# Optimization experiments

Hardware: AMD Instinct MI355X
Metric: run time of the kernel (lower is better)

## Reference

```python
import jax, jax.numpy as jnp
import numpy as np

D_MODEL = 2048
N_HEADS = 16
KV_HEADS = 4
HEAD_DIM = D_MODEL // N_HEADS  # 128
B, T = 2, 2048


def setup_inputs() -> dict:
    key = jax.random.key(0)
    ks = jax.random.split(key, 8)
    s = 1.0 / np.sqrt(D_MODEL)
    x = jax.random.normal(ks[0], (B, T, D_MODEL), dtype=jnp.float32)
    # Linear weights stored as (in_features, out_features); y = x @ W
    Wq = jax.random.normal(ks[1], (D_MODEL, D_MODEL), dtype=jnp.float32) * s
    Wk = jax.random.normal(ks[2], (D_MODEL, KV_HEADS * HEAD_DIM), dtype=jnp.float32) * s
    Wv = jax.random.normal(ks[3], (D_MODEL, KV_HEADS * HEAD_DIM), dtype=jnp.float32) * s
    Wo = jax.random.normal(ks[4], (D_MODEL, D_MODEL), dtype=jnp.float32) * s
    weight_logits = jnp.ones((KV_HEADS,), dtype=jnp.float32)
    weight_values = jnp.ones((KV_HEADS,), dtype=jnp.float32)
    # additive causal mask (1, 1, T, T): 0 on/below diag, -inf above
    neg_inf = jnp.float32(-1e30)
    causal = jnp.tril(jnp.ones((T, T), dtype=bool))
    attn_mask = jnp.where(causal, jnp.float32(0.0), neg_inf)[None, None]
    return {"x": x, "attn_mask": attn_mask, "Wq": Wq, "Wk": Wk, "Wv": Wv,
            "Wo": Wo, "weight_logits": weight_logits, "weight_values": weight_values}


def reference(x, attn_mask, Wq, Wk, Wv, Wo, weight_logits, weight_values):
    Bx, Tx, _ = x.shape
    H, G, D = N_HEADS, KV_HEADS, HEAD_DIM
    group_size = H // G
    head_to_group = jnp.arange(H) // group_size  # (H,)

    q = (x @ Wq).reshape(Bx, Tx, H, D).transpose(0, 2, 1, 3)  # (B,H,T,D)
    k = (x @ Wk).reshape(Bx, Tx, G, D).transpose(0, 2, 1, 3)  # (B,G,T,D)
    v = (x @ Wv).reshape(Bx, Tx, G, D).transpose(0, 2, 1, 3)  # (B,G,T,D)

    # GQA expansion: gather kv groups per head
    k_g = k[:, head_to_group]  # (B,H,T,D)
    v_g = v[:, head_to_group]  # (B,H,T,D)
    # (use_value_weight=False: weight_values unused)

    logit_scale = weight_logits[head_to_group][None, :, None, None]  # (1,H,1,1)
    inv_sqrt_d = jnp.float32(1.0 / np.sqrt(D))
    logits = jnp.einsum('bhqd,bhkd->bhqk', q, k_g) * inv_sqrt_d * logit_scale
    logits = logits + attn_mask
    attn = jax.nn.softmax(logits, axis=-1)  # dropout p=0 -> identity
    y = jnp.einsum('bhqk,bhkd->bhqd', attn, v_g)
    y = y.transpose(0, 2, 1, 3).reshape(Bx, Tx, H * D)
    return y @ Wo
```

## Files before the change

kernel.cpp:

```cpp
#include <hip/hip_runtime.h>
#include <hip/hip_bf16.h>

#define TT 2048
#define DM 2048
#define NH 16
#define KVH 4
#define HD 128

typedef __attribute__((ext_vector_type(8))) short bs8;
typedef __attribute__((ext_vector_type(4))) float fx4;
typedef __attribute__((ext_vector_type(4))) unsigned short us4;
typedef __attribute__((ext_vector_type(8))) unsigned short us8;

#if __has_builtin(__builtin_amdgcn_exp2f)
#define EXP2(x) __builtin_amdgcn_exp2f(x)
#else
#define EXP2(x) exp2f(x)
#endif

__device__ inline unsigned short f2b(float f) {
  __hip_bfloat16 h = __float2bfloat16(f);
  return *reinterpret_cast<unsigned short*>(&h);
}

__device__ inline float b2f(unsigned short u) {
  unsigned int v = ((unsigned int)u) << 16;
  return *reinterpret_cast<float*>(&v);
}

__device__ inline void gld_lds16(const ushort* g, ushort* l) {
  __builtin_amdgcn_global_load_lds(
      (const __attribute__((address_space(1))) void*)g,
      (__attribute__((address_space(3))) void*)l,
      16, 0, 0);
}

__global__ __launch_bounds__(256) void prep_kernel(
    const float* __restrict__ x, const float* __restrict__ Wq,
    const float* __restrict__ Wk, const float* __restrict__ Wv,
    const float* __restrict__ Wo, ushort* __restrict__ xb,
    ushort* __restrict__ Wqkvt, ushort* __restrict__ Wot) {
  int tx = threadIdx.x, ty = threadIdx.y;
  if (blockIdx.z == 2) {
    int lin = (blockIdx.y * 96 + blockIdx.x) * 256 + ty * 32 + tx;
#pragma unroll
    for (int it = 0; it < 2; ++it) {
      int i = lin + it * (6144 * 256);
      if (i < (TT * 2 * DM) / 4) {
        float4 v = ((const float4*)x)[i];
        us4 o = {f2b(v.x), f2b(v.y), f2b(v.z), f2b(v.w)};
        ((us4*)xb)[i] = o;
      }
    }
    return;
  }
  __shared__ float t[32][33];
  int n0 = blockIdx.x * 32, k0 = blockIdx.y * 32;
  if (blockIdx.z == 0) {
    const float* src;
    int srcN, col0;
    if (n0 < 2048) { src = Wq; srcN = 2048; col0 = n0; }
    else if (n0 < 2560) { src = Wk; srcN = 512; col0 = n0 - 2048; }
    else { src = Wv; srcN = 512; col0 = n0 - 2560; }
    for (int jj = 0; jj < 4; ++jj)
      t[ty + jj * 8][tx] = src[(size_t)(k0 + ty + jj * 8) * srcN + col0 + tx];
    __syncthreads();
    for (int jj = 0; jj < 4; ++jj)
      Wqkvt[(size_t)(n0 + ty + jj * 8) * 2048 + k0 + tx] = f2b(t[tx][ty + jj * 8]);
  } else {
    if (n0 >= 2048) return;
    for (int jj = 0; jj < 4; ++jj)
      t[ty + jj * 8][tx] = Wo[(size_t)(k0 + ty + jj * 8) * 2048 + n0 + tx];
    __syncthreads();
    for (int jj = 0; jj < 4; ++jj)
      Wot[(size_t)(n0 + ty + jj * 8) * 2048 + k0 + tx] = f2b(t[tx][ty + jj * 8]);
  }
}

#define EPI_STRIDE 136
__global__ __launch_bounds__(256) void gemm_qkv(const ushort* __restrict__ A,
                                                const ushort* __restrict__ Bt,
                                                ushort* __restrict__ qo,
                                                ushort* __restrict__ ko,
                                                ushort* __restrict__ vo,
                                                int K) {
  __shared__ alignas(16) ushort smem[128 * EPI_STRIDE];
  ushort* As = smem;
  ushort* Bs = smem + 8192;
  const int tid = threadIdx.x;
  const int lane = tid & 63;
  const int wid = tid >> 6;
  const int wm = wid >> 1, wn = wid & 1;
  const int quad = lane >> 4, l16 = lane & 15;
  const int bm = blockIdx.y * 128, bn = blockIdx.x * 128;

  fx4 acc[4][4];
  for (int i = 0; i < 4; ++i)
    for (int j = 0; j < 4; ++j) acc[i][j] = (fx4){0.f, 0.f, 0.f, 0.f};

  const int r8 = lane >> 3, s8 = lane & 7;
  for (int k0 = 0; k0 < K; k0 += 64) {
    for (int i = 0; i < 4; ++i) {
      int m = i * 32 + wid * 8 + r8;
      int c = s8 ^ (m & 7);
      gld_lds16(A + (size_t)(bm + m) * K + k0 + c * 8, As + (i * 32 + wid * 8) * 64);
      gld_lds16(Bt + (size_t)(bn + m) * K + k0 + c * 8, Bs + (i * 32 + wid * 8) * 64);
    }
    __syncthreads();
    for (int ks = 0; ks < 2; ++ks) {
      bs8 af[4], bf[4];
      for (int mt = 0; mt < 4; ++mt) {
        int m = wm * 64 + mt * 16 + l16;
        int c = ks * 4 + quad;
        int slot = c ^ (m & 7);
        af[mt] = *(const bs8*)(As + m * 64 + slot * 8);
      }
      for (int nt = 0; nt < 4; ++nt) {
        int n = wn * 64 + nt * 16 + l16;
        int c = ks * 4 + quad;
        int slot = c ^ (n & 7);
        bf[nt] = *(const bs8*)(Bs + n * 64 + slot * 8);
      }
      for (int mt = 0; mt < 4; ++mt)
        for (int nt = 0; nt < 4; ++nt)
          acc[mt][nt] = __builtin_amdgcn_mfma_f32_16x16x32_bf16(af[mt], bf[nt],
                                                                acc[mt][nt], 0, 0, 0);
    }
    __syncthreads();
  }

  for (int mt = 0; mt < 4; ++mt)
    for (int nt = 0; nt < 4; ++nt)
      for (int r = 0; r < 4; ++r) {
        int row = wm * 64 + mt * 16 + quad * 4 + r;
        int col = wn * 64 + nt * 16 + l16;
        smem[row * EPI_STRIDE + col] = f2b(acc[mt][nt][r]);
      }
  __syncthreads();
  const int rsel = tid >> 4;
  const int csel = tid & 15;
  for (int ii = 0; ii < 8; ++ii) {
    int row = ii * 16 + rsel;
    us8 chunk = *(const us8*)(smem + row * EPI_STRIDE + csel * 8);
    int row_g = bm + row;
    int colc = bn + csel * 8;
    if (bn < 2048) {
      *(us8*)(qo + (size_t)row_g * 2048 + colc) = chunk;
    } else {
      int b = row_g >> 11, t = row_g & 2047;
      if (bn < 2560) {
        int kc = colc - 2048;
        int gg = kc >> 7, d = kc & 127;
        *(us8*)(ko + ((size_t)(b * KVH + gg) * TT + t) * HD + d) = chunk;
      } else {
        int vc = colc - 2560;
        int gg = vc >> 7, d = vc & 127;
        *(us8*)(vo + ((size_t)(b * KVH + gg) * TT + t) * HD + d) = chunk;
      }
    }
  }
}

__global__ __launch_bounds__(256) void transpose_v(const ushort* __restrict__ vin,
                                                   ushort* __restrict__ vout) {
  __shared__ ushort tl[32][33];
  int tx = threadIdx.x, ty = threadIdx.y;
  int t0 = blockIdx.x * 32, d0 = blockIdx.y * 32;
  size_t base = (size_t)blockIdx.z * TT * HD;
  for (int jj = 0; jj < 4; ++jj)
    tl[ty + jj * 8][tx] = vin[base + (size_t)(t0 + ty + jj * 8) * HD + d0 + tx];
  __syncthreads();
  for (int jj = 0; jj < 4; ++jj)
    vout[base + (size_t)(d0 + ty + jj * 8) * TT + t0 + tx] = tl[tx][ty + jj * 8];
}

__global__ __launch_bounds__(256) void gemm_out(const ushort* __restrict__ A,
                                                const ushort* __restrict__ Bt,
                                                float* __restrict__ Cout,
                                                int N, int K) {
  __shared__ alignas(16) ushort smem[128 * EPI_STRIDE];
  ushort* As = smem;
  ushort* Bs = smem + 8192;
  const int tid = threadIdx.x;
  const int lane = tid & 63;
  const int wid = tid >> 6;
  const int wm = wid >> 1, wn = wid & 1;
  const int quad = lane >> 4, l16 = lane & 15;
  const int bm = blockIdx.y * 128, bn = blockIdx.x * 128;

  fx4 acc[4][4];
  for (int i = 0; i < 4; ++i)
    for (int j = 0; j < 4; ++j) acc[i][j] = (fx4){0.f, 0.f, 0.f, 0.f};

  const int r8 = lane >> 3, s8 = lane & 7;
  for (int k0 = 0; k0 < K; k0 += 64) {
    for (int i = 0; i < 4; ++i) {
      int m = i * 32 + wid * 8 + r8;
      int c = s8 ^ (m & 7);
      gld_lds16(A + (size_t)(bm + m) * K + k0 + c * 8, As + (i * 32 + wid * 8) * 64);
      gld_lds16(Bt + (size_t)(bn + m) * K + k0 + c * 8, Bs + (i * 32 + wid * 8) * 64);
    }
    __syncthreads();
    for (int ks = 0; ks < 2; ++ks) {
      bs8 af[4], bf[4];
      for (int mt = 0; mt < 4; ++mt) {
        int m = wm * 64 + mt * 16 + l16;
        int c = ks * 4 + quad;
        int slot = c ^ (m & 7);
        af[mt] = *(const bs8*)(As + m * 64 + slot * 8);
      }
      for (int nt = 0; nt < 4; ++nt) {
        int n = wn * 64 + nt * 16 + l16;
        int c = ks * 4 + quad;
        int slot = c ^ (n & 7);
        bf[nt] = *(const bs8*)(Bs + n * 64 + slot * 8);
      }
      for (int mt = 0; mt < 4; ++mt)
        for (int nt = 0; nt < 4; ++nt)
          acc[mt][nt] = __builtin_amdgcn_mfma_f32_16x16x32_bf16(af[mt], bf[nt],
                                                                acc[mt][nt], 0, 0, 0);
    }
    __syncthreads();
  }

  for (int mt = 0; mt < 4; ++mt)
    for (int nt = 0; nt < 4; ++nt)
      for (int r = 0; r < 4; ++r) {
        int row = wm * 64 + mt * 16 + quad * 4 + r;
        int col = wn * 64 + nt * 16 + l16;
        smem[row * EPI_STRIDE + col] = f2b(acc[mt][nt][r]);
      }
  __syncthreads();
  const int rsel = tid >> 4;
  const int csel = tid & 15;
  for (int ii = 0; ii < 8; ++ii) {
    int row = ii * 16 + rsel;
    us8 chunk = *(const us8*)(smem + row * EPI_STRIDE + csel * 8);
    int row_g = bm + row;
    int colc = bn + csel * 8;
    float4 lo = {b2f(chunk[0]), b2f(chunk[1]), b2f(chunk[2]), b2f(chunk[3])};
    float4 hi = {b2f(chunk[4]), b2f(chunk[5]), b2f(chunk[6]), b2f(chunk[7])};
    *(float4*)(Cout + (size_t)row_g * N + colc) = lo;
    *(float4*)(Cout + (size_t)row_g * N + colc + 4) = hi;
  }
}

__global__ __launch_bounds__(512, 4) void attn_kernel(const ushort* __restrict__ qb,
                                                      const ushort* __restrict__ kb,
                                                      const ushort* __restrict__ vt,
                                                      ushort* __restrict__ yb,
                                                      const float* __restrict__ wlog) {
  __shared__ alignas(16) ushort Ks[2][64 * 128];
  __shared__ alignas(16) ushort Vs[2][128 * 64];
  __shared__ alignas(16) ushort Ps[128 * 64];

  const int bid = blockIdx.x;
  const int qt = (bid & 256) ? (bid & 15) : 15 - (bid & 15);
  const int h = (bid >> 4) & 15;
  const int b = bid >> 8;
  const int g = h >> 2;
  const int tid = threadIdx.x;
  const int lane = tid & 63;
  const int wid = tid >> 6;
  const int quad = lane >> 4;
  const int l16 = lane & 15;
  const int qw = qt * 128 + wid * 16;

  const float scale = wlog[g] * 0.08838834764831845f;
  const float sc2 = scale * 1.4426950408889634f;

  const ushort* kbase = kb + (size_t)(b * KVH + g) * TT * HD;
  const ushort* vbase = vt + (size_t)(b * KVH + g) * HD * TT;

  const ushort* kp;
  const ushort* vp;
  {
    int keyr = wid * 4 + (lane >> 4);
    int si = lane & 15;
    int ck = (si & 8) | ((si ^ keyr) & 7);
    kp = kbase + (size_t)keyr * HD + ck * 8;
    int dr = wid * 8 + (lane >> 3);
    int s8 = lane & 7;
    int cv = s8 ^ (dr & 7);
    vp = vbase + (size_t)dr * TT + cv * 8;
  }

  gld_lds16(kp, &Ks[0][wid * 512]);
  gld_lds16(kp + 32 * HD, &Ks[0][4096 + wid * 512]);
  gld_lds16(vp, &Vs[0][wid * 512]);
  gld_lds16(vp + 64 * TT, &Vs[0][4096 + wid * 512]);
  kp += 64 * HD;
  vp += 64;

  bs8 qf[4];
  {
    int q = qw + l16;
    const ushort* qrow = qb + ((size_t)(b * TT + q)) * DM + h * HD;
#pragma unroll
    for (int ks = 0; ks < 4; ++ks)
      qf[ks] = *(const bs8*)(qrow + ks * 32 + quad * 8);
  }

  float m_i = -INFINITY;
  float l_i = 0.f;
  fx4 o[8];
#pragma unroll
  for (int i = 0; i < 8; ++i) o[i] = (fx4){0.f, 0.f, 0.f, 0.f};

  const int jmax = 2 * qt + 1;
  for (int j = 0; j <= jmax; ++j) {
    const int cur = j & 1;
    if (j < jmax) {
      const int nxt = cur ^ 1;
      gld_lds16(kp, &Ks[nxt][wid * 512]);
      gld_lds16(kp + 32 * HD, &Ks[nxt][4096 + wid * 512]);
      gld_lds16(vp, &Vs[nxt][wid * 512]);
      gld_lds16(vp + 64 * TT, &Vs[nxt][4096 + wid * 512]);
      kp += 64 * HD;
      vp += 64;
      asm volatile("s_waitcnt vmcnt(4)" ::: "memory");
    } else {
      asm volatile("s_waitcnt vmcnt(0)" ::: "memory");
    }
    __builtin_amdgcn_s_barrier();

    if (j * 64 <= qw + 15) {
      const ushort* Kc = Ks[cur];
      const ushort* Vc = Vs[cur];
      fx4 s[4];
#pragma unroll
      for (int mt = 0; mt < 4; ++mt) s[mt] = (fx4){0.f, 0.f, 0.f, 0.f};
      __builtin_amdgcn_s_setprio(1);
#pragma unroll
      for (int mt = 0; mt < 4; ++mt) {
        bs8 a[4];
        int key = mt * 16 + l16;
#pragma unroll
        for (int ks = 0; ks < 4; ++ks) {
          int c = ks * 4 + quad;
          int slot = (c & 8) | ((c ^ key) & 7);
          a[ks] = *(const bs8*)(Kc + key * 128 + slot * 8);
        }
#pragma unroll
        for (int ks = 0; ks < 4; ++ks)
          s[mt] = __builtin_amdgcn_mfma_f32_16x16x32_bf16(a[ks], qf[ks],
                                                          s[mt], 0, 0, 0);
      }
      __builtin_amdgcn_s_setprio(0);

      const int q = qw + l16;
      if (j * 64 + 63 > qw) {
#pragma unroll
        for (int mt = 0; mt < 4; ++mt)
#pragma unroll
          for (int r = 0; r < 4; ++r) {
            int key = j * 64 + mt * 16 + quad * 4 + r;
            if (key > q) s[mt][r] = -1e30f;
          }
      }
      float mx = s[0][0];
#pragma unroll
      for (int mt = 0; mt < 4; ++mt)
#pragma unroll
        for (int r = 0; r < 4; ++r) mx = fmaxf(mx, s[mt][r]);
      mx = fmaxf(mx, __shfl_xor(mx, 16));
      mx = fmaxf(mx, __shfl_xor(mx, 32));

      if (!__all((mx - m_i) * scale <= 8.0f)) {
        float m_new = fmaxf(m_i, mx);
        float alpha = EXP2((m_i - m_new) * sc2);
        l_i *= alpha;
#pragma unroll
        for (int dmt = 0; dmt < 8; ++dmt)
#pragma unroll
          for (int r = 0; r < 4; ++r) o[dmt][r] *= alpha;
        m_i = m_new;
      }
      float negb = -m_i * sc2;
      float sum = 0.f;
#pragma unroll
      for (int mt = 0; mt < 4; ++mt)
#pragma unroll
        for (int r = 0; r < 4; ++r) {
          float pv = EXP2(fmaf(s[mt][r], sc2, negb));
          s[mt][r] = pv;
          sum += pv;
        }
      sum += __shfl_xor(sum, 16);
      sum += __shfl_xor(sum, 32);
      l_i += sum;

      int qrow = wid * 16 + l16;
      int sw = qrow & 7;
#pragma unroll
      for (int mt = 0; mt < 4; ++mt) {
        us4 pw = {f2b(s[mt][0]), f2b(s[mt][1]), f2b(s[mt][2]), f2b(s[mt][3])};
        int chunk = mt * 2 + (quad >> 1);
        *(us4*)(Ps + qrow * 64 + ((chunk ^ sw) << 3) + ((quad & 1) << 2)) = pw;
      }

#pragma unroll
      for (int ks = 0; ks < 2; ++ks) {
        bs8 pb = *(const bs8*)(Ps + qrow * 64 + (((ks * 4 + quad) ^ sw) << 3));
        __builtin_amdgcn_s_setprio(1);
#pragma unroll
        for (int dmt = 0; dmt < 8; ++dmt) {
          int d = dmt * 16 + l16;
          int c = ks * 4 + quad;
          int slot = c ^ (d & 7);
          bs8 va = *(const bs8*)(Vc + d * 64 + slot * 8);
          o[dmt] = __builtin_amdgcn_mfma_f32_16x16x32_bf16(va, pb, o[dmt], 0, 0, 0);
        }
        __builtin_amdgcn_s_setprio(0);
      }
    }
    asm volatile("s_waitcnt lgkmcnt(0)" ::: "memory");
    __builtin_amdgcn_s_barrier();
  }

  {
    float inv = 1.0f / l_i;
    int q = qw + l16;
    ushort* yrow = yb + ((size_t)(b * TT + q)) * DM + h * HD;
#pragma unroll
    for (int dmt = 0; dmt < 8; ++dmt) {
      us4 w = {f2b(o[dmt][0] * inv), f2b(o[dmt][1] * inv),
               f2b(o[dmt][2] * inv), f2b(o[dmt][3] * inv)};
      *(us4*)(yrow + dmt * 16 + quad * 4) = w;
    }
  }
}

extern "C" void kernel_launch(void* const* d_in, const int* in_sizes, int n_in,
                              void* d_out, int out_size, void* d_ws, size_t ws_size,
                              hipStream_t stream) {
  const float* x = (const float*)d_in[0];
  const float* Wq = (const float*)d_in[2];
  const float* Wk = (const float*)d_in[3];
  const float* Wv = (const float*)d_in[4];
  const float* Wo = (const float*)d_in[5];
  const float* wlog = (const float*)d_in[6];

  char* ws = (char*)d_ws;
  ushort* xb = (ushort*)ws;     ws += (size_t)4096 * 2048 * 2;
  ushort* Wqkvt = (ushort*)ws;  ws += (size_t)3072 * 2048 * 2;
  ushort* Wot = (ushort*)ws;    ws += (size_t)2048 * 2048 * 2;
  ushort* qbuf = (ushort*)ws;   ws += (size_t)4096 * 2048 * 2;
  ushort* kbuf = (ushort*)ws;   ws += (size_t)2 * KVH * 2048 * 128 * 2;
  ushort* vtmp = (ushort*)ws;   ws += (size_t)2 * KVH * 2048 * 128 * 2;
  ushort* vbuf = (ushort*)ws;   ws += (size_t)2 * KVH * 2048 * 128 * 2;
  ushort* ybuf = (ushort*)ws;   ws += (size_t)4096 * 2048 * 2;

  prep_kernel<<<dim3(96, 64, 3), dim3(32, 8), 0, stream>>>(
      x, Wq, Wk, Wv, Wo, xb, Wqkvt, Wot);
  gemm_qkv<<<dim3(24, 32), 256, 0, stream>>>(xb, Wqkvt, qbuf, kbuf, vtmp, 2048);
  transpose_v<<<dim3(64, 4, 8), dim3(32, 8), 0, stream>>>(vtmp, vbuf);
  attn_kernel<<<512, 512, 0, stream>>>(qbuf, kbuf, vbuf, ybuf, wlog);
  gemm_out<<<dim3(16, 32), 256, 0, stream>>>(ybuf, Wot, (float*)d_out, 2048, 2048);
}
```

Before: 301.8 us.

## Give each attention wave two 16-row query tiles to reuse K/V fragments

The attention kernel moves from 8 waves of 16 query rows each to 4 waves of 32 query rows each, so every K and V fragment read from LDS feeds two MFMAs. Each thread now issues twice as many global-to-LDS loads per tile, and the vmcnt wait is adjusted to match. LDS read traffic per MFMA drops, but register pressure roughly doubles for accumulators and scores. Occupancy changes with the new launch bounds, and each causal-diagonal tile now has coarser masking per wave.

```diff
diff --git a/kernel.cpp b/kernel.cpp
--- a/kernel.cpp
+++ b/kernel.cpp
@@ -245,7 +245,7 @@
   }
 }
 
-__global__ __launch_bounds__(512, 4) void attn_kernel(const ushort* __restrict__ qb,
+__global__ __launch_bounds__(256, 2) void attn_kernel(const ushort* __restrict__ qb,
                                                       const ushort* __restrict__ kb,
                                                       const ushort* __restrict__ vt,
                                                       ushort* __restrict__ yb,
@@ -264,7 +264,7 @@
   const int wid = tid >> 6;
   const int quad = lane >> 4;
   const int l16 = lane & 15;
-  const int qw = qt * 128 + wid * 16;
+  const int qwv = qt * 128 + wid * 32;
 
   const float scale = wlog[g] * 0.08838834764831845f;
   const float sc2 = scale * 1.4426950408889634f;
@@ -285,123 +285,151 @@
     vp = vbase + (size_t)dr * TT + cv * 8;
   }
 
-  gld_lds16(kp, &Ks[0][wid * 512]);
-  gld_lds16(kp + 32 * HD, &Ks[0][4096 + wid * 512]);
-  gld_lds16(vp, &Vs[0][wid * 512]);
-  gld_lds16(vp + 64 * TT, &Vs[0][4096 + wid * 512]);
+#pragma unroll
+  for (int r = 0; r < 4; ++r) {
+    gld_lds16(kp + (size_t)(16 * r) * HD, &Ks[0][r * 2048 + wid * 512]);
+    gld_lds16(vp + (size_t)(32 * r) * TT, &Vs[0][r * 2048 + wid * 512]);
+  }
   kp += 64 * HD;
   vp += 64;
 
-  bs8 qf[4];
-  {
-    int q = qw + l16;
+  bs8 qf[2][4];
+#pragma unroll
+  for (int nt = 0; nt < 2; ++nt) {
+    int q = qwv + nt * 16 + l16;
     const ushort* qrow = qb + ((size_t)(b * TT + q)) * DM + h * HD;
 #pragma unroll
     for (int ks = 0; ks < 4; ++ks)
-      qf[ks] = *(const bs8*)(qrow + ks * 32 + quad * 8);
-  }
-
-  float m_i = -INFINITY;
-  float l_i = 0.f;
-  fx4 o[8];
-#pragma unroll
-  for (int i = 0; i < 8; ++i) o[i] = (fx4){0.f, 0.f, 0.f, 0.f};
+      qf[nt][ks] = *(const bs8*)(qrow + ks * 32 + quad * 8);
+  }
+
+  float m_i[2] = {-INFINITY, -INFINITY};
+  float l_i[2] = {0.f, 0.f};
+  fx4 o[8][2];
+#pragma unroll
+  for (int i = 0; i < 8; ++i)
+#pragma unroll
+    for (int nt = 0; nt < 2; ++nt) o[i][nt] = (fx4){0.f, 0.f, 0.f, 0.f};
 
   const int jmax = 2 * qt + 1;
   for (int j = 0; j <= jmax; ++j) {
     const int cur = j & 1;
     if (j < jmax) {
       const int nxt = cur ^ 1;
-      gld_lds16(kp, &Ks[nxt][wid * 512]);
-      gld_lds16(kp + 32 * HD, &Ks[nxt][4096 + wid * 512]);
-      gld_lds16(vp, &Vs[nxt][wid * 512]);
-      gld_lds16(vp + 64 * TT, &Vs[nxt][4096 + wid * 512]);
+#pragma unroll
+      for (int r = 0; r < 4; ++r) {
+        gld_lds16(kp + (size_t)(16 * r) * HD, &Ks[nxt][r * 2048 + wid * 512]);
+        gld_lds16(vp + (size_t)(32 * r) * TT, &Vs[nxt][r * 2048 + wid * 512]);
+      }
       kp += 64 * HD;
       vp += 64;
-      asm volatile("s_waitcnt vmcnt(4)" ::: "memory");
+      asm volatile("s_waitcnt vmcnt(8)" ::: "memory");
     } else {
       asm volatile("s_waitcnt vmcnt(0)" ::: "memory");
     }
     __builtin_amdgcn_s_barrier();
 
-    if (j * 64 <= qw + 15) {
+    if (j * 64 <= qwv + 31) {
       const ushort* Kc = Ks[cur];
       const ushort* Vc = Vs[cur];
-      fx4 s[4];
-#pragma unroll
-      for (int mt = 0; mt < 4; ++mt) s[mt] = (fx4){0.f, 0.f, 0.f, 0.f};
+      fx4 s[4][2];
+#pragma unroll
+      for (int mt = 0; mt < 4; ++mt)
+#pragma unroll
+        for (int nt = 0; nt < 2; ++nt) s[mt][nt] = (fx4){0.f, 0.f, 0.f, 0.f};
       __builtin_amdgcn_s_setprio(1);
 #pragma unroll
       for (int mt = 0; mt < 4; ++mt) {
-        bs8 a[4];
         int key = mt * 16 + l16;
 #pragma unroll
         for (int ks = 0; ks < 4; ++ks) {
           int c = ks * 4 + quad;
           int slot = (c & 8) | ((c ^ key) & 7);
-          a[ks] = *(const bs8*)(Kc + key * 128 + slot * 8);
+          bs8 a = *(const bs8*)(Kc + key * 128 + slot * 8);
+          s[mt][0] = __builtin_amdgcn_mfma_f32_16x16x32_bf16(a, qf[0][ks],
+                                                             s[mt][0], 0, 0, 0);
+          s[mt][1] = __builtin_amdgcn_mfma_f32_16x16x32_bf16(a, qf[1][ks],
+                                                             s[mt][1], 0, 0, 0);
         }
-#pragma unroll
-        for (int ks = 0; ks < 4; ++ks)
-          s[mt] = __builtin_amdgcn_mfma_f32_16x16x32_bf16(a[ks], qf[ks],
-                                                          s[mt], 0, 0, 0);
       }
       __builtin_amdgcn_s_setprio(0);
 
-      const int q = qw + l16;
-      if (j * 64 + 63 > qw) {
+      if (j * 64 + 63 > qwv) {
+#pragma unroll
+        for (int nt = 0; nt < 2; ++nt) {
+          int q = qwv + nt * 16 + l16;
+#pragma unroll
+          for (int mt = 0; mt < 4; ++mt)
+#pragma unroll
+            for (int r = 0; r < 4; ++r) {
+              int key = j * 64 + mt * 16 + quad * 4 + r;
+              if (key > q) s[mt][nt][r] = -1e30f;
+            }
+        }
+      }
+      float mx[2];
+#pragma unroll
+      for (int nt = 0; nt < 2; ++nt) {
+        float m = s[0][nt][0];
 #pragma unroll
         for (int mt = 0; mt < 4; ++mt)
 #pragma unroll
+          for (int r = 0; r < 4; ++r) m = fmaxf(m, s[mt][nt][r]);
+        m = fmaxf(m, __shfl_xor(m, 16));
+        m = fmaxf(m, __shfl_xor(m, 32));
+        mx[nt] = m;
+      }
+
+      bool ok = ((mx[0] - m_i[0]) * scale <= 8.0f) &&
+                ((mx[1] - m_i[1]) * scale <= 8.0f);
+      if (!__all(ok)) {
+#pragma unroll
+        for (int nt = 0; nt < 2; ++nt) {
+          float m_new = fmaxf(m_i[nt], mx[nt]);
+          float alpha = EXP2((m_i[nt] - m_new) * sc2);
+          l_i[nt] *= alpha;
+#pragma unroll
+          for (int dmt = 0; dmt < 8; ++dmt)
+#pragma unroll
+            for (int r = 0; r < 4; ++r) o[dmt][nt][r] *= alpha;
+          m_i[nt] = m_new;
+        }
+      }
+#pragma unroll
+      for (int nt = 0; nt < 2; ++nt) {
+        float negb = -m_i[nt] * sc2;
+        float sum = 0.f;
+#pragma unroll
+        for (int mt = 0; mt < 4; ++mt)
+#pragma unroll
           for (int r = 0; r < 4; ++r) {
-            int key = j * 64 + mt * 16 + quad * 4 + r;
-            if (key > q) s[mt][r] = -1e30f;
+            float pv = EXP2(fmaf(s[mt][nt][r], sc2, negb));
+            s[mt][nt][r] = pv;
+            sum += pv;
           }
-      }
-      float mx = s[0][0];
-#pragma unroll
-      for (int mt = 0; mt < 4; ++mt)
-#pragma unroll
-        for (int r = 0; r < 4; ++r) mx = fmaxf(mx, s[mt][r]);
-      mx = fmaxf(mx, __shfl_xor(mx, 16));
-      mx = fmaxf(mx, __shfl_xor(mx, 32));
-
-      if (!__all((mx - m_i) * scale <= 8.0f)) {
-        float m_new = fmaxf(m_i, mx);
-        float alpha = EXP2((m_i - m_new) * sc2);
-        l_i *= alpha;
-#pragma unroll
-        for (int dmt = 0; dmt < 8; ++dmt)
-#pragma unroll
-          for (int r = 0; r < 4; ++r) o[dmt][r] *= alpha;
-        m_i = m_new;
-      }
-      float negb = -m_i * sc2;
-      float sum = 0.f;
-#pragma unroll
-      for (int mt = 0; mt < 4; ++mt)
-#pragma unroll
-        for (int r = 0; r < 4; ++r) {
-          float pv = EXP2(fmaf(s[mt][r], sc2, negb));
-          s[mt][r] = pv;
-          sum += pv;
+        sum += __shfl_xor(sum, 16);
+        sum += __shfl_xor(sum, 32);
+        l_i[nt] += sum;
+      }
+
+      const int sw = l16 & 7;
+#pragma unroll
+      for (int nt = 0; nt < 2; ++nt) {
+        int qrow = wid * 32 + nt * 16 + l16;
+#pragma unroll
+        for (int mt = 0; mt < 4; ++mt) {
+          us4 pw = {f2b(s[mt][nt][0]), f2b(s[mt][nt][1]),
+                    f2b(s[mt][nt][2]), f2b(s[mt][nt][3])};
+          int chunk = mt * 2 + (quad >> 1);
+          *(us4*)(Ps + qrow * 64 + ((chunk ^ sw) << 3) + ((quad & 1) << 2)) = pw;
         }
-      sum += __shfl_xor(sum, 16);
-      sum += __shfl_xor(sum, 32);
-      l_i += sum;
-
-      int qrow = wid * 16 + l16;
-      int sw = qrow & 7;
-#pragma unroll
-      for (int mt = 0; mt < 4; ++mt) {
-        us4 pw = {f2b(s[mt][0]), f2b(s[mt][1]), f2b(s[mt][2]), f2b(s[mt][3])};
-        int chunk = mt * 2 + (quad >> 1);
-        *(us4*)(Ps + qrow * 64 + ((chunk ^ sw) << 3) + ((quad & 1) << 2)) = pw;
       }
 
 #pragma unroll
       for (int ks = 0; ks < 2; ++ks) {
-        bs8 pb = *(const bs8*)(Ps + qrow * 64 + (((ks * 4 + quad) ^ sw) << 3));
+        int qrow0 = wid * 32 + l16;
+        bs8 pb0 = *(const bs8*)(Ps + qrow0 * 64 + (((ks * 4 + quad) ^ sw) << 3));
+        bs8 pb1 = *(const bs8*)(Ps + (qrow0 + 16) * 64 + (((ks * 4 + quad) ^ sw) << 3));
         __builtin_amdgcn_s_setprio(1);
 #pragma unroll
         for (int dmt = 0; dmt < 8; ++dmt) {
@@ -409,7 +437,8 @@
           int c = ks * 4 + quad;
           int slot = c ^ (d & 7);
           bs8 va = *(const bs8*)(Vc + d * 64 + slot * 8);
-          o[dmt] = __builtin_amdgcn_mfma_f32_16x16x32_bf16(va, pb, o[dmt], 0, 0, 0);
+          o[dmt][0] = __builtin_amdgcn_mfma_f32_16x16x32_bf16(va, pb0, o[dmt][0], 0, 0, 0);
+          o[dmt][1] = __builtin_amdgcn_mfma_f32_16x16x32_bf16(va, pb1, o[dmt][1], 0, 0, 0);
         }
         __builtin_amdgcn_s_setprio(0);
       }
@@ -418,14 +447,15 @@
     __builtin_amdgcn_s_barrier();
   }
 
-  {
-    float inv = 1.0f / l_i;
-    int q = qw + l16;
+#pragma unroll
+  for (int nt = 0; nt < 2; ++nt) {
+    float inv = 1.0f / l_i[nt];
+    int q = qwv + nt * 16 + l16;
     ushort* yrow = yb + ((size_t)(b * TT + q)) * DM + h * HD;
 #pragma unroll
     for (int dmt = 0; dmt < 8; ++dmt) {
-      us4 w = {f2b(o[dmt][0] * inv), f2b(o[dmt][1] * inv),
-               f2b(o[dmt][2] * inv), f2b(o[dmt][3] * inv)};
+      us4 w = {f2b(o[dmt][nt][0] * inv), f2b(o[dmt][nt][1] * inv),
+               f2b(o[dmt][nt][2] * inv), f2b(o[dmt][nt][3] * inv)};
       *(us4*)(yrow + dmt * 16 + quad * 4) = w;
     }
   }
@@ -455,6 +485,6 @@
       x, Wq, Wk, Wv, Wo, xb, Wqkvt, Wot);
   gemm_qkv<<<dim3(24, 32), 256, 0, stream>>>(xb, Wqkvt, qbuf, kbuf, vtmp, 2048);
   transpose_v<<<dim3(64, 4, 8), dim3(32, 8), 0, stream>>>(vtmp, vbuf);
-  attn_kernel<<<512, 512, 0, stream>>>(qbuf, kbuf, vbuf, ybuf, wlog);
+  attn_kernel<<<512, 256, 0, stream>>>(qbuf, kbuf, vbuf, ybuf, wlog);
   gemm_out<<<dim3(16, 32), 256, 0, stream>>>(ybuf, Wot, (float*)d_out, 2048, 2048);
 }
```

Measured after the change: 305.1 us. No clear change (+1.1%).

## Load V fragments directly from global memory and reorder blocks for KV-group locality

Applied to the files above, without the earlier changes.

V tiles are no longer staged through shared memory. Each wave reads its V^T fragments straight from global memory into registers, in two halves of eight bs8 loads per key block. The block index mapping is also changed so that consecutive blocks share the same batch and KV group, which should improve L2 reuse of K and V. This cuts LDS traffic and halves shared memory use, which could raise occupancy. In exchange, every wave issues redundant global loads for V, and their latency is only partly hidden behind the QK MFMAs.

```diff
diff --git a/kernel.cpp b/kernel.cpp
--- a/kernel.cpp
+++ b/kernel.cpp
@@ -251,14 +251,16 @@
                                                       ushort* __restrict__ yb,
                                                       const float* __restrict__ wlog) {
   __shared__ alignas(16) ushort Ks[2][64 * 128];
-  __shared__ alignas(16) ushort Vs[2][128 * 64];
   __shared__ alignas(16) ushort Ps[128 * 64];
 
   const int bid = blockIdx.x;
-  const int qt = (bid & 256) ? (bid & 15) : 15 - (bid & 15);
-  const int h = (bid >> 4) & 15;
-  const int b = bid >> 8;
-  const int g = h >> 2;
+  const int b = bid & 1;
+  const int g = (bid >> 1) & 3;
+  const int i = bid >> 3;
+  const int hi = i >> 4;
+  const int lo = i & 15;
+  const int qt = (hi & 2) ? (15 - lo) : lo;
+  const int h = g * 4 + hi;
   const int tid = threadIdx.x;
   const int lane = tid & 63;
   const int wid = tid >> 6;
@@ -273,24 +275,17 @@
   const ushort* vbase = vt + (size_t)(b * KVH + g) * HD * TT;
 
   const ushort* kp;
-  const ushort* vp;
   {
     int keyr = wid * 4 + (lane >> 4);
     int si = lane & 15;
     int ck = (si & 8) | ((si ^ keyr) & 7);
     kp = kbase + (size_t)keyr * HD + ck * 8;
-    int dr = wid * 8 + (lane >> 3);
-    int s8 = lane & 7;
-    int cv = s8 ^ (dr & 7);
-    vp = vbase + (size_t)dr * TT + cv * 8;
-  }
+  }
+  const ushort* vrow = vbase + (size_t)l16 * TT + quad * 8;
 
   gld_lds16(kp, &Ks[0][wid * 512]);
   gld_lds16(kp + 32 * HD, &Ks[0][4096 + wid * 512]);
-  gld_lds16(vp, &Vs[0][wid * 512]);
-  gld_lds16(vp + 64 * TT, &Vs[0][4096 + wid * 512]);
   kp += 64 * HD;
-  vp += 64;
 
   bs8 qf[4];
   {
@@ -305,7 +300,7 @@
   float l_i = 0.f;
   fx4 o[8];
 #pragma unroll
-  for (int i = 0; i < 8; ++i) o[i] = (fx4){0.f, 0.f, 0.f, 0.f};
+  for (int i2 = 0; i2 < 8; ++i2) o[i2] = (fx4){0.f, 0.f, 0.f, 0.f};
 
   const int jmax = 2 * qt + 1;
   for (int j = 0; j <= jmax; ++j) {
@@ -314,11 +309,8 @@
       const int nxt = cur ^ 1;
       gld_lds16(kp, &Ks[nxt][wid * 512]);
       gld_lds16(kp + 32 * HD, &Ks[nxt][4096 + wid * 512]);
-      gld_lds16(vp, &Vs[nxt][wid * 512]);
-      gld_lds16(vp + 64 * TT, &Vs[nxt][4096 + wid * 512]);
       kp += 64 * HD;
-      vp += 64;
-      asm volatile("s_waitcnt vmcnt(4)" ::: "memory");
+      asm volatile("s_waitcnt vmcnt(2)" ::: "memory");
     } else {
       asm volatile("s_waitcnt vmcnt(0)" ::: "memory");
     }
@@ -326,7 +318,12 @@
 
     if (j * 64 <= qw + 15) {
       const ushort* Kc = Ks[cur];
-      const ushort* Vc = Vs[cur];
+      const ushort* vj = vrow + j * 64;
+      bs8 vf[8];
+#pragma unroll
+      for (int dmt = 0; dmt < 8; ++dmt)
+        vf[dmt] = *(const bs8*)(vj + (size_t)(dmt * 16) * TT);
+
       fx4 s[4];
 #pragma unroll
       for (int mt = 0; mt < 4; ++mt) s[mt] = (fx4){0.f, 0.f, 0.f, 0.f};
@@ -391,7 +388,7 @@
       l_i += sum;
 
       int qrow = wid * 16 + l16;
-      int sw = qrow & 7;
+      int sw = l16 & 7;
 #pragma unroll
       for (int mt = 0; mt < 4; ++mt) {
         us4 pw = {f2b(s[mt][0]), f2b(s[mt][1]), f2b(s[mt][2]), f2b(s[mt][3])};
@@ -399,18 +396,23 @@
         *(us4*)(Ps + qrow * 64 + ((chunk ^ sw) << 3) + ((quad & 1) << 2)) = pw;
       }
 
-#pragma unroll
-      for (int ks = 0; ks < 2; ++ks) {
-        bs8 pb = *(const bs8*)(Ps + qrow * 64 + (((ks * 4 + quad) ^ sw) << 3));
+      {
+        bs8 pb = *(const bs8*)(Ps + qrow * 64 + (((0 * 4 + quad) ^ sw) << 3));
         __builtin_amdgcn_s_setprio(1);
 #pragma unroll
-        for (int dmt = 0; dmt < 8; ++dmt) {
-          int d = dmt * 16 + l16;
-          int c = ks * 4 + quad;
-          int slot = c ^ (d & 7);
-          bs8 va = *(const bs8*)(Vc + d * 64 + slot * 8);
-          o[dmt] = __builtin_amdgcn_mfma_f32_16x16x32_bf16(va, pb, o[dmt], 0, 0, 0);
-        }
+        for (int dmt = 0; dmt < 8; ++dmt)
+          o[dmt] = __builtin_amdgcn_mfma_f32_16x16x32_bf16(vf[dmt], pb, o[dmt], 0, 0, 0);
+        __builtin_amdgcn_s_setprio(0);
+      }
+#pragma unroll
+      for (int dmt = 0; dmt < 8; ++dmt)
+        vf[dmt] = *(const bs8*)(vj + (size_t)(dmt * 16) * TT + 32);
+      {
+        bs8 pb = *(const bs8*)(Ps + qrow * 64 + (((1 * 4 + quad) ^ sw) << 3));
+        __builtin_amdgcn_s_setprio(1);
+#pragma unroll
+        for (int dmt = 0; dmt < 8; ++dmt)
+          o[dmt] = __builtin_amdgcn_mfma_f32_16x16x32_bf16(vf[dmt], pb, o[dmt], 0, 0, 0);
         __builtin_amdgcn_s_setprio(0);
       }
     }
```

Measured after the change: 385.8 us. 27.8% more time.
